# Optimization experiments

Hardware: AMD Instinct MI355X
Metric: run time of the kernel (lower is better)

The kernel has to match this reference:

```python
import jax, jax.numpy as jnp
import numpy as np

B, C, H, W = 16, 256, 64, 64
HEADS, KK, UU, M = 4, 16, 1, 7
OUT_CH = 256
VV = OUT_CH // HEADS  # 64
PAD = (M - 1) // 2
EPS = 1e-5


def group_norm(x, gamma, beta, groups):
    # x: [B, Cc, H, W]; normalize per (group, spatial) like torch GroupNorm
    b, c, h, w = x.shape
    xg = x.reshape(b, groups, c // groups, h, w)
    mu = xg.mean(axis=(2, 3, 4), keepdims=True)
    var = xg.var(axis=(2, 3, 4), keepdims=True)
    xn = ((xg - mu) * jax.lax.rsqrt(var + EPS)).reshape(b, c, h, w)
    return xn * gamma[None, :, None, None] + beta[None, :, None, None]


def setup_inputs() -> dict:
    key = jax.random.key(0)
    ks = jax.random.split(key, 5)
    x = jax.random.normal(ks[0], (B, C, H, W), dtype=jnp.float32)
    # 1x1 conv weights (out_ch, in_ch); kaiming-ish scale
    s = 1.0 / np.sqrt(C)
    wq = jax.random.normal(ks[1], (KK * HEADS, C), dtype=jnp.float32) * s
    wk = jax.random.normal(ks[2], (KK * UU, C), dtype=jnp.float32) * s
    wv = jax.random.normal(ks[3], (VV * UU, C), dtype=jnp.float32) * s
    embedding = jax.random.normal(ks[4], (KK, UU, 1, M, M), dtype=jnp.float32)
    return {
        "x": x,
        "wq": wq, "gq_gamma": jnp.ones((KK * HEADS,), jnp.float32), "gq_beta": jnp.zeros((KK * HEADS,), jnp.float32),
        "wk": wk, "gk_gamma": jnp.ones((KK * UU,), jnp.float32), "gk_beta": jnp.zeros((KK * UU,), jnp.float32),
        "wv": wv, "gv_gamma": jnp.ones((VV * UU,), jnp.float32), "gv_beta": jnp.zeros((VV * UU,), jnp.float32),
        "embedding": embedding,
    }


def reference(x, wq, gq_gamma, gq_beta, wk, gk_gamma, gk_beta, wv, gv_gamma, gv_beta, embedding):
    b, _, h, w = x.shape
    n = h * w
    # 1x1 conv projections + GroupNorm
    q = group_norm(jnp.einsum('bchw,oc->bohw', x, wq), gq_gamma, gq_beta, KK * HEADS // 4)
    q = q.reshape(b, HEADS, KK, n)                                     # bhkn
    k_ = group_norm(jnp.einsum('bchw,oc->bohw', x, wk), gk_gamma, gk_beta, KK * UU // 4)
    k_sm = jax.nn.softmax(k_.reshape(b, KK, UU, n), axis=-1)           # bkun, softmax over positions
    v = group_norm(jnp.einsum('bchw,oc->bohw', x, wv), gv_gamma, gv_beta, VV * UU // 4)
    v = v.reshape(b, VV, UU, n)                                        # bvun
    # content lambda
    lam_c = jnp.einsum('bkun,bvun->bkv', k_sm, v)
    content = jnp.einsum('bhkn,bkv->bhvn', q, lam_c)
    # position lambda: conv3d over values reinterpreted as [B, UU, VV, H, W]
    v3 = v.reshape(b, UU, VV, h, w)  # matches torch .view (uu=1 so pure reinterpretation)
    ctx = jax.lax.conv_general_dilated(
        v3, embedding, window_strides=(1, 1, 1),
        padding=[(0, 0), (PAD, PAD), (PAD, PAD)],
        dimension_numbers=('NCDHW', 'OIDHW', 'NCDHW'))                  # [B, KK, VV, H, W]
    ctx = ctx.reshape(b, KK, VV, n)
    context = jnp.einsum('bhkn,bkvn->bhvn', q, ctx)
    out = (content + context).reshape(b, HEADS * VV, h, w)
    return out
```

## Files before the change

### kernel.cpp

```cpp
#include <hip/hip_runtime.h>
#include <math.h>

#define B_    16
#define C_    256
#define H_    64
#define W_    64
#define N_    4096
#define HEADS_ 4
#define KK_   16
#define VV_   64
#define M_    7
#define PAD_  3
#define OTOT_ 144
#define NG_   36
#define EPS_  1e-5f

typedef __attribute__((ext_vector_type(8))) short short8b;
typedef __attribute__((ext_vector_type(4))) float f32x4;

__device__ inline unsigned packbf(float a, float b) {
  unsigned ua = __float_as_uint(a) + 0x8000u;
  unsigned ub = __float_as_uint(b) + 0x8000u;
  return (ua >> 16) | (ub & 0xffff0000u);
}
__device__ inline float bflo(unsigned u) { return __uint_as_float(u << 16); }
__device__ inline float bfhi(unsigned u) { return __uint_as_float(u & 0xffff0000u); }

__global__ __launch_bounds__(256) void k_wcvt(const float* __restrict__ wq,
    const float* __restrict__ wk, const float* __restrict__ wv,
    unsigned short* __restrict__ wbf) {
  const int idx = blockIdx.x * 256 + threadIdx.x;
  if (idx >= OTOT_ * C_) return;
  const int o = idx >> 8, c = idx & 255;
  const float* wrow = (o < 64) ? (wq + o * C_)
                     : ((o < 80) ? (wk + (o - 64) * C_) : (wv + (o - 80) * C_));
  wbf[idx] = (unsigned short)((__float_as_uint(wrow[c]) + 0x8000u) >> 16);
}

__global__ __launch_bounds__(256) void k_proj_mfma(const float* __restrict__ x,
    const unsigned short* __restrict__ wbf, float* __restrict__ proj) {
  const int pt = blockIdx.x;
  const int b  = blockIdx.y;
  const int px0 = pt * 64;
  const int tid = threadIdx.x;
  const int w    = tid >> 6;
  const int lane = tid & 63;
  const int ln15 = lane & 15;
  const int lg   = lane >> 4;

  __shared__ unsigned short s_x[2][2048];

  const int spx = tid & 63;
  const int skg = tid >> 6;
  const float* xb = x + (size_t)b * C_ * N_ + px0 + spx;

  f32x4 acc[9];
  #pragma unroll
  for (int t = 0; t < 9; ++t) acc[t] = (f32x4){0.f, 0.f, 0.f, 0.f};

  for (int step = 0; step < 8; ++step) {
    const int c0  = step * 32;
    const int buf = step & 1;
    {
      float v[8];
      #pragma unroll
      for (int j = 0; j < 8; ++j)
        v[j] = xb[(size_t)(c0 + skg * 8 + j) * N_];
      uint4 u;
      u.x = packbf(v[0], v[1]);
      u.y = packbf(v[2], v[3]);
      u.z = packbf(v[4], v[5]);
      u.w = packbf(v[6], v[7]);
      *reinterpret_cast<uint4*>(&s_x[buf][skg * 512 + spx * 8]) = u;
    }
    __syncthreads();
    const short8b bfrag = *reinterpret_cast<const short8b*>(
        &s_x[buf][lg * 512 + (w * 16 + ln15) * 8]);
    #pragma unroll
    for (int ot = 0; ot < 9; ++ot) {
      const short8b afrag = *reinterpret_cast<const short8b*>(
          wbf + (size_t)(ot * 16 + ln15) * C_ + c0 + lg * 8);
      acc[ot] = __builtin_amdgcn_mfma_f32_16x16x32_bf16(afrag, bfrag, acc[ot], 0, 0, 0);
    }
  }

  float* pb = proj + (size_t)b * OTOT_ * N_ + px0 + w * 16 + ln15;
  #pragma unroll
  for (int ot = 0; ot < 9; ++ot)
    #pragma unroll
    for (int r = 0; r < 4; ++r)
      pb[(size_t)(ot * 16 + lg * 4 + r) * N_] = acc[ot][r];
}

__global__ __launch_bounds__(256) void k_stats(const float* __restrict__ proj,
    float* __restrict__ meanp, float* __restrict__ rstdp) {
  const int bg = blockIdx.x;
  const int b = bg / NG_, g = bg % NG_;
  const float* p = proj + ((size_t)b * OTOT_ + g * 4) * N_;
  float s = 0.f, s2 = 0.f;
  for (int i = threadIdx.x * 4; i < 4 * N_; i += 1024) {
    const float4 v = *reinterpret_cast<const float4*>(p + i);
    s  += v.x + v.y + v.z + v.w;
    s2 += v.x * v.x + v.y * v.y + v.z * v.z + v.w * v.w;
  }
  __shared__ float rs[256], rq[256];
  rs[threadIdx.x] = s; rq[threadIdx.x] = s2;
  __syncthreads();
  for (int off = 128; off > 0; off >>= 1) {
    if (threadIdx.x < off) {
      rs[threadIdx.x] += rs[threadIdx.x + off];
      rq[threadIdx.x] += rq[threadIdx.x + off];
    }
    __syncthreads();
  }
  if (threadIdx.x == 0) {
    float m   = rs[0] * (1.f / 16384.f);
    float var = rq[0] * (1.f / 16384.f) - m * m;
    meanp[bg] = m;
    rstdp[bg] = rsqrtf(var + EPS_);
  }
}

__global__ __launch_bounds__(256) void k_softmax(const float* __restrict__ proj,
    const float* __restrict__ meanp, const float* __restrict__ rstdp,
    const float* __restrict__ gkg, const float* __restrict__ gkb,
    float* __restrict__ ksm) {
  const int bk = blockIdx.x;
  const int b = bk >> 4, kk = bk & 15;
  const int g = 16 + (kk >> 2);
  const float mu = meanp[b * NG_ + g], rs = rstdp[b * NG_ + g];
  const float ga = gkg[kk], be = gkb[kk];
  const float* p = proj + ((size_t)b * OTOT_ + 64 + kk) * N_;
  float* o = ksm + ((size_t)b * KK_ + kk) * N_;

  float xn[16];
  float m = -1e30f;
  #pragma unroll
  for (int i = 0; i < 16; ++i) {
    float v = (p[threadIdx.x + i * 256] - mu) * rs * ga + be;
    xn[i] = v;
    m = fmaxf(m, v);
  }
  __shared__ float red[256];
  red[threadIdx.x] = m; __syncthreads();
  for (int off = 128; off > 0; off >>= 1) {
    if (threadIdx.x < off)
      red[threadIdx.x] = fmaxf(red[threadIdx.x], red[threadIdx.x + off]);
    __syncthreads();
  }
  m = red[0];
  __syncthreads();
  float s = 0.f;
  #pragma unroll
  for (int i = 0; i < 16; ++i) { xn[i] = __expf(xn[i] - m); s += xn[i]; }
  red[threadIdx.x] = s; __syncthreads();
  for (int off = 128; off > 0; off >>= 1) {
    if (threadIdx.x < off) red[threadIdx.x] += red[threadIdx.x + off];
    __syncthreads();
  }
  float inv = 1.f / red[0];
  #pragma unroll
  for (int i = 0; i < 16; ++i) o[threadIdx.x + i * 256] = xn[i] * inv;
}

__global__ __launch_bounds__(256) void k_lam(const float* __restrict__ proj,
    const float* __restrict__ ksm,
    const float* __restrict__ meanp, const float* __restrict__ rstdp,
    const float* __restrict__ gvg, const float* __restrict__ gvb,
    float* __restrict__ lam) {
  const int bv = blockIdx.x;
  const int b = bv >> 6, v = bv & 63;
  const int g = 20 + (v >> 2);
  const float mu = meanp[b * NG_ + g], rs = rstdp[b * NG_ + g];
  const float ga = gvg[v], be = gvb[v];
  const float* pv = proj + ((size_t)b * OTOT_ + 80 + v) * N_;
  const float* pk = ksm + (size_t)b * KK_ * N_;

  float acc[16];
  #pragma unroll
  for (int k = 0; k < 16; ++k) acc[k] = 0.f;
  for (int n = threadIdx.x * 4; n < N_; n += 1024) {
    float4 vn = *reinterpret_cast<const float4*>(pv + n);
    vn.x = (vn.x - mu) * rs * ga + be;
    vn.y = (vn.y - mu) * rs * ga + be;
    vn.z = (vn.z - mu) * rs * ga + be;
    vn.w = (vn.w - mu) * rs * ga + be;
    #pragma unroll
    for (int k = 0; k < 16; ++k) {
      const float4 kv = *reinterpret_cast<const float4*>(pk + (size_t)k * N_ + n);
      acc[k] += kv.x * vn.x + kv.y * vn.y + kv.z * vn.z + kv.w * vn.w;
    }
  }
  __shared__ float red[64];
  const int lane = threadIdx.x & 63, wid = threadIdx.x >> 6;
  #pragma unroll
  for (int k = 0; k < 16; ++k) {
    float s = acc[k];
    #pragma unroll
    for (int off = 32; off > 0; off >>= 1) s += __shfl_down(s, off, 64);
    if (lane == 0) red[wid * 16 + k] = s;
  }
  __syncthreads();
  if (threadIdx.x < 16) {
    float s = red[threadIdx.x] + red[16 + threadIdx.x] +
              red[32 + threadIdx.x] + red[48 + threadIdx.x];
    lam[((size_t)b * KK_ + threadIdx.x) * VV_ + v] = s;
  }
}

__global__ __launch_bounds__(256) void k_qe(const float* __restrict__ proj,
    const float* __restrict__ meanp, const float* __restrict__ rstdp,
    const float* __restrict__ gqg, const float* __restrict__ gqb,
    const float* __restrict__ emb, unsigned short* __restrict__ qeb) {
  const int strip = blockIdx.x;
  const int h     = blockIdx.y;
  const int b     = blockIdx.z;
  const int r0    = strip * 4;
  const int tid   = threadIdx.x;
  const int wid   = __builtin_amdgcn_readfirstlane(tid >> 6);
  const int slot  = tid & 63;
  const int ty    = slot >> 4, txg = slot & 15;
  const int x0    = txg << 2;
  const int n0    = (r0 + ty) * W_ + x0;

  const float* pb = proj + (size_t)b * OTOT_ * N_;

  float qn[4][16];
  #pragma unroll
  for (int k = 0; k < 16; ++k) {
    const int o = h * 16 + k, g = o >> 2;
    const float mu = meanp[b * NG_ + g], rs = rstdp[b * NG_ + g];
    const float ga = gqg[o], be = gqb[o];
    const float4 qv = *reinterpret_cast<const float4*>(pb + (size_t)o * N_ + n0);
    qn[0][k] = (qv.x - mu) * rs * ga + be;
    qn[1][k] = (qv.y - mu) * rs * ga + be;
    qn[2][k] = (qv.z - mu) * rs * ga + be;
    qn[3][k] = (qv.w - mu) * rs * ga + be;
  }

  unsigned short* qb = qeb + (size_t)(b * 4 + h) * 49 * N_;
  const int t0 = wid * 13;
  const int t1 = (t0 + 13 < 49) ? (t0 + 13) : 49;
  for (int t = t0; t < t1; ++t) {
    float p0 = 0.f, p1 = 0.f, p2 = 0.f, p3 = 0.f;
    #pragma unroll
    for (int k = 0; k < 16; ++k) {
      const float e = emb[k * 49 + t];
      p0 += qn[0][k] * e; p1 += qn[1][k] * e;
      p2 += qn[2][k] * e; p3 += qn[3][k] * e;
    }
    uint2 pk;
    pk.x = packbf(p0, p1);
    pk.y = packbf(p2, p3);
    *reinterpret_cast<uint2*>(&qb[(size_t)t * N_ + n0]) = pk;
  }
}

__global__ __launch_bounds__(256) void k_final_v10(const float* __restrict__ proj,
    const float* __restrict__ meanp, const float* __restrict__ rstdp,
    const float* __restrict__ gqg, const float* __restrict__ gqb,
    const float* __restrict__ gvg, const float* __restrict__ gvb,
    const unsigned short* __restrict__ qeb, const float* __restrict__ lam,
    float* __restrict__ out) {
  const int wgid = (blockIdx.x & 7) * 1024 + (blockIdx.x >> 3);
  const int b     = wgid >> 9;
  const int r2    = wgid & 511;
  const int h     = r2 & 3;
  const int strip = (r2 >> 2) & 15;
  const int s     = r2 >> 6;

  const int r0    = strip * 4;
  const int tid   = threadIdx.x;
  const int vlane = __builtin_amdgcn_readfirstlane(tid >> 6);
  const int slot  = tid & 63;
  const int ty    = slot >> 4;
  const int txg   = slot & 15;
  const int x0    = txg << 2;
  const int n0    = (r0 + ty) * W_ + x0;
  const int pos4  = ty * 64 + x0;

  __shared__ unsigned short s_qe[49 * 256];
  __shared__ unsigned short s_v[8 * 720];
  __shared__ float s_mu[NG_], s_rs[NG_];
  __shared__ float s_gvw[64], s_gvb[64];

  if (tid < NG_) { s_mu[tid] = meanp[b * NG_ + tid]; s_rs[tid] = rstdp[b * NG_ + tid]; }
  else if (tid >= 64 && tid < 128) { s_gvw[tid - 64] = gvg[tid - 64]; s_gvb[tid - 64] = gvb[tid - 64]; }
  for (int i = tid; i < 160; i += 256) {
    const int vh = i / 20, rem = i % 20;
    const int ry = rem >> 1, side = rem & 1;
    uint2 z; z.x = 0u; z.y = 0u;
    *reinterpret_cast<uint2*>(&s_v[vh * 720 + ry * 72 + side * 68]) = z;
  }
  __syncthreads();

  const float* pb = proj + (size_t)b * OTOT_ * N_;

  {
    const unsigned short* qb = qeb + (size_t)(b * 4 + h) * 49 * N_ + r0 * 64;
    for (int i = tid; i < 1568; i += 256) {
      const int t = i >> 5;
      const int r = i & 31;
      const uint4 d = *reinterpret_cast<const uint4*>(&qb[(size_t)t * N_ + r * 8]);
      *reinterpret_cast<uint4*>(&s_qe[t * 256 + r * 8]) = d;
    }
  }

  {
    const int half = tid >> 7;
    const int vh   = (tid >> 4) & 7;
    const int rx4  = (tid & 15) + 1;
    const int gx0  = (rx4 << 2) - 4;
    const int v    = s * 8 + vh;
    const int g    = 20 + (v >> 2);
    const float mu = s_mu[g], rs = s_rs[g], ga = s_gvw[v], be = s_gvb[v];
    const float* src = pb + (size_t)(80 + v) * N_ + gx0;
    unsigned short* dst = &s_v[vh * 720 + (rx4 << 2)];
    #pragma unroll
    for (int rr = 0; rr < 5; ++rr) {
      const int ry = half * 5 + rr;
      const int gy = r0 - 3 + ry;
      float4 f = make_float4(0.f, 0.f, 0.f, 0.f);
      if (gy >= 0 && gy < H_) {
        f = *reinterpret_cast<const float4*>(src + (size_t)gy * W_);
        f.x = (f.x - mu) * rs * ga + be;
        f.y = (f.y - mu) * rs * ga + be;
        f.z = (f.z - mu) * rs * ga + be;
        f.w = (f.w - mu) * rs * ga + be;
      }
      uint2 w;
      w.x = packbf(f.x, f.y);
      w.y = packbf(f.z, f.w);
      *reinterpret_cast<uint2*>(dst + ry * 72) = w;
    }
  }
  __syncthreads();

  float acc[2][4];
  #pragma unroll
  for (int vj = 0; vj < 2; ++vj)
    #pragma unroll
    for (int p = 0; p < 4; ++p) acc[vj][p] = 0.f;

  const float* lb = lam + (size_t)b * 1024;
  #pragma unroll
  for (int k = 0; k < 16; ++k) {
    const int o = h * 16 + k, g = o >> 2;
    const float mu = s_mu[g], rs = s_rs[g];
    const float ga = gqg[o], be = gqb[o];
    const float4 qv = *reinterpret_cast<const float4*>(pb + (size_t)o * N_ + n0);
    const float q0 = (qv.x - mu) * rs * ga + be;
    const float q1 = (qv.y - mu) * rs * ga + be;
    const float q2 = (qv.z - mu) * rs * ga + be;
    const float q3 = (qv.w - mu) * rs * ga + be;
    #pragma unroll
    for (int vj = 0; vj < 2; ++vj) {
      const int v = __builtin_amdgcn_readfirstlane(s * 8 + vj * 4 + vlane);
      const float lv = lb[k * 64 + v];
      acc[vj][0] += q0 * lv; acc[vj][1] += q1 * lv;
      acc[vj][2] += q2 * lv; acc[vj][3] += q3 * lv;
    }
  }

  #pragma unroll
  for (int i = 0; i < 7; ++i) {
    float qeu[7][4];
    #pragma unroll
    for (int j = 0; j < 7; ++j) {
      const uint2 pk = *reinterpret_cast<const uint2*>(&s_qe[(i * 7 + j) * 256 + pos4]);
      qeu[j][0] = bflo(pk.x); qeu[j][1] = bfhi(pk.x);
      qeu[j][2] = bflo(pk.y); qeu[j][3] = bfhi(pk.y);
    }
    #pragma unroll
    for (int vj = 0; vj < 2; ++vj) {
      const int vh = vj * 4 + vlane;
      const unsigned short* sv = &s_v[vh * 720 + (ty + i) * 72 + x0];
      const uint2 wa = *reinterpret_cast<const uint2*>(sv);
      const uint2 wb = *reinterpret_cast<const uint2*>(sv + 4);
      const uint2 wc = *reinterpret_cast<const uint2*>(sv + 8);
      float wv[12];
      wv[0] = bflo(wa.x); wv[1] = bfhi(wa.x); wv[2]  = bflo(wa.y); wv[3]  = bfhi(wa.y);
      wv[4] = bflo(wb.x); wv[5] = bfhi(wb.x); wv[6]  = bflo(wb.y); wv[7]  = bfhi(wb.y);
      wv[8] = bflo(wc.x); wv[9] = bfhi(wc.x); wv[10] = bflo(wc.y); wv[11] = bfhi(wc.y);
      #pragma unroll
      for (int j = 0; j < 7; ++j)
        #pragma unroll
        for (int p = 0; p < 4; ++p)
          acc[vj][p] += qeu[j][p] * wv[p + j + 1];
    }
  }

  #pragma unroll
  for (int vj = 0; vj < 2; ++vj) {
    const int v = s * 8 + vj * 4 + vlane;
    float4 o4 = make_float4(acc[vj][0], acc[vj][1], acc[vj][2], acc[vj][3]);
    *reinterpret_cast<float4*>(out + ((size_t)b * 256 + h * 64 + v) * N_ + n0) = o4;
  }
}

extern "C" void kernel_launch(void* const* d_in, const int* in_sizes, int n_in,
                              void* d_out, int out_size, void* d_ws, size_t ws_size,
                              hipStream_t stream) {
  const float* x   = (const float*)d_in[0];
  const float* wq  = (const float*)d_in[1];
  const float* gqg = (const float*)d_in[2];
  const float* gqb = (const float*)d_in[3];
  const float* wk  = (const float*)d_in[4];
  const float* gkg = (const float*)d_in[5];
  const float* gkb = (const float*)d_in[6];
  const float* wv  = (const float*)d_in[7];
  const float* gvg = (const float*)d_in[8];
  const float* gvb = (const float*)d_in[9];
  const float* emb = (const float*)d_in[10];
  float* out = (float*)d_out;
  float* ws  = (float*)d_ws;

  float* proj  = ws;
  float* meanp = proj + (size_t)B_ * OTOT_ * N_;
  float* rstdp = meanp + B_ * NG_;
  float* ksm   = rstdp + B_ * NG_;
  float* lam   = ksm + (size_t)B_ * KK_ * N_;
  unsigned short* qeb = (unsigned short*)(lam + (size_t)B_ * KK_ * VV_);
  unsigned short* wbf = qeb + (size_t)B_ * HEADS_ * 49 * N_;

  k_wcvt<<<dim3(144), 256, 0, stream>>>(wq, wk, wv, wbf);
  k_proj_mfma<<<dim3(64, B_), 256, 0, stream>>>(x, wbf, proj);
  k_stats<<<dim3(B_ * NG_), 256, 0, stream>>>(proj, meanp, rstdp);
  k_softmax<<<dim3(B_ * KK_), 256, 0, stream>>>(proj, meanp, rstdp, gkg, gkb, ksm);
  k_lam<<<dim3(B_ * VV_), 256, 0, stream>>>(proj, ksm, meanp, rstdp, gvg, gvb, lam);
  k_qe<<<dim3(16, HEADS_, B_), 256, 0, stream>>>(proj, meanp, rstdp, gqg, gqb, emb, qeb);
  k_final_v10<<<dim3(8192), 256, 0, stream>>>(proj, meanp, rstdp,
      gqg, gqb, gvg, gvb, qeb, lam, out);
}
```

Before: 169.0 us.

## Halve per-block value channels in final kernel and prefetch x in projection

The final kernel now gives each block 4 value channels instead of 8, which doubles the grid to 16384 blocks, halves the s_v shared buffer and cuts per-thread accumulators. This may raise occupancy and parallelism, but each block still stages the full 49x256 qe tile, so qe global traffic and the q normalization work per output are doubled. The projection kernel also prefetches the next x chunk into registers before the MFMA loop so the global load latency can overlap with compute.

Result: slower. 196.6 us (+16.3%).

```diff
diff --git a/kernel.cpp b/kernel.cpp
--- a/kernel.cpp
+++ b/kernel.cpp
@@ -58,20 +58,26 @@
   #pragma unroll
   for (int t = 0; t < 9; ++t) acc[t] = (f32x4){0.f, 0.f, 0.f, 0.f};
 
+  float vx[8];
+  #pragma unroll
+  for (int j = 0; j < 8; ++j) vx[j] = xb[(size_t)(skg * 8 + j) * N_];
+
   for (int step = 0; step < 8; ++step) {
     const int c0  = step * 32;
     const int buf = step & 1;
     {
-      float v[8];
+      uint4 u;
+      u.x = packbf(vx[0], vx[1]);
+      u.y = packbf(vx[2], vx[3]);
+      u.z = packbf(vx[4], vx[5]);
+      u.w = packbf(vx[6], vx[7]);
+      *reinterpret_cast<uint4*>(&s_x[buf][skg * 512 + spx * 8]) = u;
+    }
+    float vn[8];
+    if (step < 7) {
+      const int c1 = c0 + 32;
       #pragma unroll
-      for (int j = 0; j < 8; ++j)
-        v[j] = xb[(size_t)(c0 + skg * 8 + j) * N_];
-      uint4 u;
-      u.x = packbf(v[0], v[1]);
-      u.y = packbf(v[2], v[3]);
-      u.z = packbf(v[4], v[5]);
-      u.w = packbf(v[6], v[7]);
-      *reinterpret_cast<uint4*>(&s_x[buf][skg * 512 + spx * 8]) = u;
+      for (int j = 0; j < 8; ++j) vn[j] = xb[(size_t)(c1 + skg * 8 + j) * N_];
     }
     __syncthreads();
     const short8b bfrag = *reinterpret_cast<const short8b*>(
@@ -81,6 +87,10 @@
       const short8b afrag = *reinterpret_cast<const short8b*>(
           wbf + (size_t)(ot * 16 + ln15) * C_ + c0 + lg * 8);
       acc[ot] = __builtin_amdgcn_mfma_f32_16x16x32_bf16(afrag, bfrag, acc[ot], 0, 0, 0);
+    }
+    if (step < 7) {
+      #pragma unroll
+      for (int j = 0; j < 8; ++j) vx[j] = vn[j];
     }
   }
 
@@ -256,15 +266,15 @@
   }
 }
 
-__global__ __launch_bounds__(256) void k_final_v10(const float* __restrict__ proj,
+__global__ __launch_bounds__(256) void k_final_v11(const float* __restrict__ proj,
     const float* __restrict__ meanp, const float* __restrict__ rstdp,
     const float* __restrict__ gqg, const float* __restrict__ gqb,
     const float* __restrict__ gvg, const float* __restrict__ gvb,
     const unsigned short* __restrict__ qeb, const float* __restrict__ lam,
     float* __restrict__ out) {
-  const int wgid = (blockIdx.x & 7) * 1024 + (blockIdx.x >> 3);
-  const int b     = wgid >> 9;
-  const int r2    = wgid & 511;
+  const int wgid = (blockIdx.x & 7) * 2048 + (blockIdx.x >> 3);
+  const int b     = wgid >> 10;
+  const int r2    = wgid & 1023;
   const int h     = r2 & 3;
   const int strip = (r2 >> 2) & 15;
   const int s     = r2 >> 6;
@@ -280,14 +290,14 @@
   const int pos4  = ty * 64 + x0;
 
   __shared__ unsigned short s_qe[49 * 256];
-  __shared__ unsigned short s_v[8 * 720];
+  __shared__ unsigned short s_v[4 * 720];
   __shared__ float s_mu[NG_], s_rs[NG_];
   __shared__ float s_gvw[64], s_gvb[64];
 
   if (tid < NG_) { s_mu[tid] = meanp[b * NG_ + tid]; s_rs[tid] = rstdp[b * NG_ + tid]; }
   else if (tid >= 64 && tid < 128) { s_gvw[tid - 64] = gvg[tid - 64]; s_gvb[tid - 64] = gvb[tid - 64]; }
-  for (int i = tid; i < 160; i += 256) {
-    const int vh = i / 20, rem = i % 20;
+  if (tid < 80) {
+    const int vh = tid / 20, rem = tid % 20;
     const int ry = rem >> 1, side = rem & 1;
     uint2 z; z.x = 0u; z.y = 0u;
     *reinterpret_cast<uint2*>(&s_v[vh * 720 + ry * 72 + side * 68]) = z;
@@ -307,59 +317,54 @@
   }
 
   {
-    const int half = tid >> 7;
-    const int vh   = (tid >> 4) & 7;
-    const int rx4  = (tid & 15) + 1;
-    const int gx0  = (rx4 << 2) - 4;
-    const int v    = s * 8 + vh;
-    const int g    = 20 + (v >> 2);
+    const int vh  = (tid >> 6) & 3;
+    const int rg  = (tid >> 4) & 3;
+    const int rx4 = (tid & 15) + 1;
+    const int gx0 = (rx4 << 2) - 4;
+    const int v   = s * 4 + vh;
+    const int g   = 20 + (v >> 2);
     const float mu = s_mu[g], rs = s_rs[g], ga = s_gvw[v], be = s_gvb[v];
     const float* src = pb + (size_t)(80 + v) * N_ + gx0;
     unsigned short* dst = &s_v[vh * 720 + (rx4 << 2)];
     #pragma unroll
-    for (int rr = 0; rr < 5; ++rr) {
-      const int ry = half * 5 + rr;
-      const int gy = r0 - 3 + ry;
-      float4 f = make_float4(0.f, 0.f, 0.f, 0.f);
-      if (gy >= 0 && gy < H_) {
-        f = *reinterpret_cast<const float4*>(src + (size_t)gy * W_);
-        f.x = (f.x - mu) * rs * ga + be;
-        f.y = (f.y - mu) * rs * ga + be;
-        f.z = (f.z - mu) * rs * ga + be;
-        f.w = (f.w - mu) * rs * ga + be;
+    for (int rr = 0; rr < 3; ++rr) {
+      const int ry = rg + 4 * rr;
+      if (ry < 10) {
+        const int gy = r0 - 3 + ry;
+        float4 f = make_float4(0.f, 0.f, 0.f, 0.f);
+        if (gy >= 0 && gy < H_) {
+          f = *reinterpret_cast<const float4*>(src + (size_t)gy * W_);
+          f.x = (f.x - mu) * rs * ga + be;
+          f.y = (f.y - mu) * rs * ga + be;
+          f.z = (f.z - mu) * rs * ga + be;
+          f.w = (f.w - mu) * rs * ga + be;
+        }
+        uint2 w;
+        w.x = packbf(f.x, f.y);
+        w.y = packbf(f.z, f.w);
+        *reinterpret_cast<uint2*>(dst + ry * 72) = w;
       }
-      uint2 w;
-      w.x = packbf(f.x, f.y);
-      w.y = packbf(f.z, f.w);
-      *reinterpret_cast<uint2*>(dst + ry * 72) = w;
     }
   }
   __syncthreads();
 
-  float acc[2][4];
-  #pragma unroll
-  for (int vj = 0; vj < 2; ++vj)
-    #pragma unroll
-    for (int p = 0; p < 4; ++p) acc[vj][p] = 0.f;
+  float acc[4];
+  #pragma unroll
+  for (int p = 0; p < 4; ++p) acc[p] = 0.f;
 
   const float* lb = lam + (size_t)b * 1024;
+  const int v_out = __builtin_amdgcn_readfirstlane(s * 4 + vlane);
   #pragma unroll
   for (int k = 0; k < 16; ++k) {
     const int o = h * 16 + k, g = o >> 2;
     const float mu = s_mu[g], rs = s_rs[g];
     const float ga = gqg[o], be = gqb[o];
     const float4 qv = *reinterpret_cast<const float4*>(pb + (size_t)o * N_ + n0);
-    const float q0 = (qv.x - mu) * rs * ga + be;
-    const float q1 = (qv.y - mu) * rs * ga + be;
-    const float q2 = (qv.z - mu) * rs * ga + be;
-    const float q3 = (qv.w - mu) * rs * ga + be;
-    #pragma unroll
-    for (int vj = 0; vj < 2; ++vj) {
-      const int v = __builtin_amdgcn_readfirstlane(s * 8 + vj * 4 + vlane);
-      const float lv = lb[k * 64 + v];
-      acc[vj][0] += q0 * lv; acc[vj][1] += q1 * lv;
-      acc[vj][2] += q2 * lv; acc[vj][3] += q3 * lv;
-    }
+    const float lv = lb[k * 64 + v_out];
+    acc[0] += ((qv.x - mu) * rs * ga + be) * lv;
+    acc[1] += ((qv.y - mu) * rs * ga + be) * lv;
+    acc[2] += ((qv.z - mu) * rs * ga + be) * lv;
+    acc[3] += ((qv.w - mu) * rs * ga + be) * lv;
   }
 
   #pragma unroll
@@ -371,10 +376,8 @@
       qeu[j][0] = bflo(pk.x); qeu[j][1] = bfhi(pk.x);
       qeu[j][2] = bflo(pk.y); qeu[j][3] = bfhi(pk.y);
     }
-    #pragma unroll
-    for (int vj = 0; vj < 2; ++vj) {
-      const int vh = vj * 4 + vlane;
-      const unsigned short* sv = &s_v[vh * 720 + (ty + i) * 72 + x0];
+    {
+      const unsigned short* sv = &s_v[vlane * 720 + (ty + i) * 72 + x0];
       const uint2 wa = *reinterpret_cast<const uint2*>(sv);
       const uint2 wb = *reinterpret_cast<const uint2*>(sv + 4);
       const uint2 wc = *reinterpret_cast<const uint2*>(sv + 8);
@@ -386,14 +389,13 @@
       for (int j = 0; j < 7; ++j)
         #pragma unroll
         for (int p = 0; p < 4; ++p)
-          acc[vj][p] += qeu[j][p] * wv[p + j + 1];
-    }
-  }
-
-  #pragma unroll
-  for (int vj = 0; vj < 2; ++vj) {
-    const int v = s * 8 + vj * 4 + vlane;
-    float4 o4 = make_float4(acc[vj][0], acc[vj][1], acc[vj][2], acc[vj][3]);
+          acc[p] += qeu[j][p] * wv[p + j + 1];
+    }
+  }
+
+  {
+    const int v = s * 4 + vlane;
+    float4 o4 = make_float4(acc[0], acc[1], acc[2], acc[3]);
     *reinterpret_cast<float4*>(out + ((size_t)b * 256 + h * 64 + v) * N_ + n0) = o4;
   }
 }
@@ -429,6 +431,6 @@
   k_softmax<<<dim3(B_ * KK_), 256, 0, stream>>>(proj, meanp, rstdp, gkg, gkb, ksm);
   k_lam<<<dim3(B_ * VV_), 256, 0, stream>>>(proj, ksm, meanp, rstdp, gvg, gvb, lam);
   k_qe<<<dim3(16, HEADS_, B_), 256, 0, stream>>>(proj, meanp, rstdp, gqg, gqb, emb, qeb);
-  k_final_v10<<<dim3(8192), 256, 0, stream>>>(proj, meanp, rstdp,
+  k_final_v11<<<dim3(16384), 256, 0, stream>>>(proj, meanp, rstdp,
       gqg, gqb, gvg, gvb, qeb, lam, out);
 }
```
